# Performance work log

Measured on AMD Instinct MI355X. Metric: run time of the kernel, lower is better.

The kernel has to match this reference:

```python
import jax, jax.numpy as jnp
import numpy as np
from jax import lax

B, C, H, W = 4, 96, 256, 256
EPS = 1e-12  # torch F.normalize default eps


def setup_inputs() -> dict:
    key = jax.random.key(0)
    ks = jax.random.split(key, 7)
    s1 = 1.0 / np.sqrt(C).astype(np.float32)
    x = jax.random.normal(ks[0], (B, C, H, W), dtype=jnp.float32)
    qkv_w = jax.random.normal(ks[1], (3 * C, C), dtype=jnp.float32) * s1      # 1x1 conv as matmul
    qkv_b = jax.random.normal(ks[2], (3 * C,), dtype=jnp.float32) * 0.01
    dw_w = jax.random.normal(ks[3], (3 * C, 1, 3, 3), dtype=jnp.float32) / 3.0  # depthwise 3x3
    dw_b = jax.random.normal(ks[4], (3 * C,), dtype=jnp.float32) * 0.01
    temp = jnp.ones((C, 1, 1), dtype=jnp.float32)                             # nn.Parameter(ones(dim,1,1))
    proj_w = jax.random.normal(ks[5], (C, C), dtype=jnp.float32) * s1
    proj_b = jax.random.normal(ks[6], (C,), dtype=jnp.float32) * 0.01
    return {"x": x, "qkv_w": qkv_w, "qkv_b": qkv_b, "dw_w": dw_w,
            "dw_b": dw_b, "temp": temp, "proj_w": proj_w, "proj_b": proj_b}


def _l2norm_h(t):
    # torch F.normalize(t, dim=-2): L2 over the H axis, eps-clamped denominator
    n = jnp.sqrt(jnp.sum(t * t, axis=-2, keepdims=True))
    return t / jnp.maximum(n, EPS)


def reference(x, qkv_w, qkv_b, dw_w, dw_b, temp, proj_w, proj_b):
    # 1x1 conv QKV projection
    qkv = jnp.einsum('bchw,oc->bohw', x, qkv_w) + qkv_b[None, :, None, None]
    # depthwise 3x3 conv (groups = 3C), padding 1
    qkv = lax.conv_general_dilated(
        qkv, dw_w, window_strides=(1, 1), padding='SAME',
        feature_group_count=qkv.shape[1],
        dimension_numbers=('NCHW', 'OIHW', 'NCHW')) + dw_b[None, :, None, None]
    q, k, v = jnp.split(qkv, 3, axis=1)  # each [B,C,H,W]
    q1 = _l2norm_h(q)
    k1 = _l2norm_h(k)
    # attn1 = (q1^T @ k1) * temperature : [B,C,W,W], temp broadcasts over (W,W)
    attn = jnp.einsum('bchw,bchv->bcwv', q1, k1) * temp[None]
    attn = jax.nn.softmax(attn, axis=-2)
    # out = v @ attn : [B,C,H,W]
    out = jnp.einsum('bchw,bcwv->bchv', v, attn)
    # 1x1 output projection
    out = jnp.einsum('bchw,oc->bohw', out, proj_w) + proj_b[None, :, None, None]
    return out
```

## Files before the change

### kernel.cpp

```cpp
#include <hip/hip_runtime.h>

#define NC 96
#define NC3 288
#define NH 256
#define NW 256
#define NHW 65536

typedef unsigned short ushort_t;
typedef __attribute__((ext_vector_type(8))) short bf16x8;
typedef __attribute__((ext_vector_type(4))) float f32x4;

__device__ __forceinline__ ushort_t f2bf(float x) {
  unsigned u = __float_as_uint(x);
  u += 0x7fffu + ((u >> 16) & 1u);
  return (ushort_t)(u >> 16);
}
__device__ __forceinline__ float bf2f(ushort_t h) {
  return __uint_as_float((unsigned)h << 16);
}
__device__ __forceinline__ unsigned pack_split(float f) {
  unsigned u = __float_as_uint(f);
  unsigned ur = u + (0x7fffu + ((u >> 16) & 1u));
  const float rem = f - __uint_as_float(ur & 0xffff0000u);
  unsigned v = __float_as_uint(rem);
  v += 0x7fffu + ((v >> 16) & 1u);
  return (ur >> 16) | (v & 0xffff0000u);
}
__device__ __forceinline__ float upk(unsigned u) {
  return __uint_as_float(u << 16) + __uint_as_float(u & 0xffff0000u);
}

__global__ __launch_bounds__(256) void k_wprep(
    const float* __restrict__ qkv_w, const float* __restrict__ proj_w,
    ushort_t* __restrict__ wq_hi, ushort_t* __restrict__ wq_lo,
    ushort_t* __restrict__ wp_hi, ushort_t* __restrict__ wp_lo) {
  const int id = blockIdx.x * 256 + threadIdx.x;
  if (id < NC3 * NC) {
    const float v = qkv_w[id];
    const ushort_t h = f2bf(v);
    wq_hi[id] = h;
    wq_lo[id] = f2bf(v - bf2f(h));
  } else {
    const int j = id - NC3 * NC;
    const float v = proj_w[j];
    const ushort_t h = f2bf(v);
    wp_hi[j] = h;
    wp_lo[j] = f2bf(v - bf2f(h));
  }
}

template <int OUTC, bool TILED>
__global__ __launch_bounds__(256, 4) void k_conv(
    const float* __restrict__ in, const ushort_t* __restrict__ w_hi,
    const ushort_t* __restrict__ w_lo, const float* __restrict__ bias,
    float* __restrict__ out) {
  __shared__ __align__(16) char smem[39936];
  ushort_t* xh = (ushort_t*)smem;
  ushort_t* xl = (ushort_t*)(smem + 13312);
  float* xt48 = (float*)(smem + 26624);
  float* est = (float*)smem;
  const int t = threadIdx.x;
  const int bz = blockIdx.y;
  const int sblk = blockIdx.x;
  const int s0 = sblk * 64;
  const float* xb = in + (size_t)bz * NC * NHW + s0;

  const int lane = t & 63, wave = t >> 6;
  const int ln15 = lane & 15;
  const int akof = (lane >> 4) * 8;

#pragma unroll 1
  for (int half = 0; half < 2; ++half) {
    if (half) __syncthreads();
#pragma unroll
    for (int i = 0; i < 3; ++i) {
      const int idx = t + 256 * i;
      const int row = idx >> 4, c4 = (idx & 15) << 2;
      *(float4*)&xt48[row * 68 + c4] =
          *(const float4*)&xb[(size_t)(half * 48 + row) * NHW + c4];
    }
    __syncthreads();
    {
      const int s = t & 63, cg = t >> 6;
#pragma unroll
      for (int i = 0; i < 6; ++i) {
        const int cl = cg * 12 + i * 2;
        const float f0 = xt48[cl * 68 + s], f1 = xt48[(cl + 1) * 68 + s];
        const ushort_t h0 = f2bf(f0), h1 = f2bf(f1);
        const ushort_t l0 = f2bf(f0 - bf2f(h0)), l1 = f2bf(f1 - bf2f(h1));
        const int c = half * 48 + cl;
        *(unsigned*)&xh[s * 104 + c] = (unsigned)h0 | ((unsigned)h1 << 16);
        *(unsigned*)&xl[s * 104 + c] = (unsigned)l0 | ((unsigned)l1 << 16);
      }
    }
  }
  __syncthreads();
  bf16x8 bH[3], bL[3];
  {
    const int srow = wave * 16 + ln15;
#pragma unroll
    for (int kk = 0; kk < 3; ++kk) {
      bH[kk] = *(const bf16x8*)&xh[srow * 104 + kk * 32 + akof];
      bL[kk] = *(const bf16x8*)&xl[srow * 104 + kk * 32 + akof];
    }
  }

  constexpr int S = 3 * (OUTC / 96);
  const int sl = wave * 16 + ln15;
  f32x4 acc[6];
#pragma unroll
  for (int step = 0; step < S; ++step) {
    const int ocg = step / 3, kk = step % 3;
    if (kk == 0) {
#pragma unroll
      for (int m = 0; m < 6; ++m) acc[m] = (f32x4){0.f, 0.f, 0.f, 0.f};
    }
#pragma unroll
    for (int m = 0; m < 6; ++m) {
      const int wi = (ocg * 96 + m * 16 + ln15) * NC + kk * 32 + akof;
      const bf16x8 aH = *(const bf16x8*)(w_hi + wi);
      const bf16x8 aL = *(const bf16x8*)(w_lo + wi);
      acc[m] = __builtin_amdgcn_mfma_f32_16x16x32_bf16(aH, bH[kk], acc[m], 0, 0, 0);
      acc[m] = __builtin_amdgcn_mfma_f32_16x16x32_bf16(aH, bL[kk], acc[m], 0, 0, 0);
      acc[m] = __builtin_amdgcn_mfma_f32_16x16x32_bf16(aL, bH[kk], acc[m], 0, 0, 0);
    }
    if (kk == 2) {
      __syncthreads();
#pragma unroll
      for (int m = 0; m < 6; ++m) {
        const int o2 = m * 16 + (lane >> 4) * 4;
#pragma unroll
        for (int r = 0; r < 4; ++r) est[(o2 + r) * 66 + sl] = acc[m][r];
      }
      __syncthreads();
      if (TILED) {
        unsigned* ob = (unsigned*)out +
                       ((size_t)(bz * 1024 + sblk)) * OUTC * 64 +
                       (size_t)ocg * 96 * 64;
#pragma unroll
        for (int j = 0; j < 6; ++j) {
          const int idx = t + 256 * j;
          const int row = idx >> 4, c4 = (idx & 15) << 2;
          const float bs = bias[ocg * 96 + row];
          uint4 pkv;
          pkv.x = pack_split(est[row * 66 + c4 + 0] + bs);
          pkv.y = pack_split(est[row * 66 + c4 + 1] + bs);
          pkv.z = pack_split(est[row * 66 + c4 + 2] + bs);
          pkv.w = pack_split(est[row * 66 + c4 + 3] + bs);
          *(uint4*)(ob + (size_t)row * 64 + c4) = pkv;
        }
      } else {
        float* ob = out + (size_t)bz * OUTC * NHW + s0;
#pragma unroll
        for (int j = 0; j < 6; ++j) {
          const int idx = t + 256 * j;
          const int row = idx >> 4, c4 = (idx & 15) << 2;
          const float bs = bias[ocg * 96 + row];
          const float4 v = make_float4(
              est[row * 66 + c4] + bs, est[row * 66 + c4 + 1] + bs,
              est[row * 66 + c4 + 2] + bs, est[row * 66 + c4 + 3] + bs);
          *(float4*)(ob + (size_t)(ocg * 96 + row) * NHW + c4) = v;
        }
      }
    }
  }
}

__global__ __launch_bounds__(256, 8) void k_dw3(
    const unsigned* __restrict__ qkvt, const float* __restrict__ w,
    const float* __restrict__ bias, ushort_t* __restrict__ qt_hi,
    ushort_t* __restrict__ qt_lo, ushort_t* __restrict__ kt_hi,
    ushort_t* __restrict__ kt_lo, unsigned* __restrict__ v_pk,
    float* __restrict__ nq_p, float* __restrict__ nk_p) {
  __shared__ float sd[18][264];
  const int t = threadIdx.x;
  const int hb = blockIdx.x;
  const int bcc = blockIdx.y;
  const int b = bcc / NC3, ch = bcc % NC3;
  const int h0 = hb * 16;
  const unsigned* src = qkvt + (size_t)b * 1024 * NC3 * 64 + (size_t)ch * 64;
#pragma unroll
  for (int i = 0; i < 5; ++i) {
    const int idx = t + 256 * i;
    if (idx < 18 * 64) {
      const int r = idx >> 6, j = idx & 63;
      const int gh = h0 + r - 1;
      float4 v = make_float4(0.f, 0.f, 0.f, 0.f);
      if (gh >= 0 && gh < 256) {
        const int gw = 4 * j;
        const uint4 pv = *(const uint4*)&src[(size_t)(gh * 4 + (gw >> 6)) *
                                                 (NC3 * 64) +
                                             (gw & 63)];
        v = make_float4(upk(pv.x), upk(pv.y), upk(pv.z), upk(pv.w));
      }
      *(float4*)&sd[r][4 + 4 * j] = v;
    }
  }
  if (t < 36) {
    const int r = t >> 1;
    sd[r][(t & 1) ? 260 : 3] = 0.f;
  }
  __syncthreads();
  float wr[9];
#pragma unroll
  for (int k = 0; k < 9; ++k) wr[k] = w[ch * 9 + k];
  const float bs = bias[ch];
  const int wl = t;
  float res[16];
  float r0a = sd[0][wl + 3], r0b = sd[0][wl + 4], r0c = sd[0][wl + 5];
  float r1a = sd[1][wl + 3], r1b = sd[1][wl + 4], r1c = sd[1][wl + 5];
#pragma unroll
  for (int r = 0; r < 16; ++r) {
    const float r2a = sd[r + 2][wl + 3], r2b = sd[r + 2][wl + 4],
                r2c = sd[r + 2][wl + 5];
    float a = bs;
    a = fmaf(r0a, wr[0], a);
    a = fmaf(r0b, wr[1], a);
    a = fmaf(r0c, wr[2], a);
    a = fmaf(r1a, wr[3], a);
    a = fmaf(r1b, wr[4], a);
    a = fmaf(r1c, wr[5], a);
    a = fmaf(r2a, wr[6], a);
    a = fmaf(r2b, wr[7], a);
    a = fmaf(r2c, wr[8], a);
    res[r] = a;
    r0a = r1a; r0b = r1b; r0c = r1c;
    r1a = r2a; r1b = r2b; r1c = r2c;
  }
  if (ch < 192) {
    const int qk = ch / 96, c = ch - qk * 96;
    const int bc = b * 96 + c;
    float ss = 0.f;
#pragma unroll
    for (int r = 0; r < 16; ++r) ss = fmaf(res[r], res[r], ss);
    (qk ? nk_p : nq_p)[(size_t)bc * 4096 + hb * 256 + wl] = ss;
    const size_t tb = (size_t)bc * NHW + (size_t)hb * 4096 + (size_t)wl * 16;
    ushort_t* dh = (qk ? kt_hi : qt_hi) + tb;
    ushort_t* dl = (qk ? kt_lo : qt_lo) + tb;
#pragma unroll
    for (int j4 = 0; j4 < 2; ++j4) {
      uint4 H, L;
      unsigned* ph = (unsigned*)&H;
      unsigned* pl = (unsigned*)&L;
#pragma unroll
      for (int e = 0; e < 4; ++e) {
        const float f0 = res[j4 * 8 + 2 * e], f1 = res[j4 * 8 + 2 * e + 1];
        const ushort_t hh0 = f2bf(f0), hh1 = f2bf(f1);
        ph[e] = (unsigned)hh0 | ((unsigned)hh1 << 16);
        pl[e] = (unsigned)f2bf(f0 - bf2f(hh0)) |
                ((unsigned)f2bf(f1 - bf2f(hh1)) << 16);
      }
      *(uint4*)(dh + j4 * 8) = H;
      *(uint4*)(dl + j4 * 8) = L;
    }
  } else {
    const int bc = b * 96 + (ch - 192);
    const int wb = wl >> 5, wsub = wl & 31;
    unsigned* dp = v_pk + (size_t)bc * NHW + wb * 8192 + wsub;
#pragma unroll
    for (int r = 0; r < 16; ++r) {
      const float f = res[r];
      const ushort_t hh = f2bf(f);
      dp[(h0 + r) * 32] = (unsigned)hh | ((unsigned)f2bf(f - bf2f(hh)) << 16);
    }
  }
}

__global__ __launch_bounds__(256, 3) void k_attn_mfma(
    const ushort_t* __restrict__ qt_hi, const ushort_t* __restrict__ qt_lo,
    const ushort_t* __restrict__ kt_hi, const ushort_t* __restrict__ kt_lo,
    const float* __restrict__ nq_p, const float* __restrict__ nk_p,
    const float* __restrict__ temp, ushort_t* __restrict__ pt_hi,
    ushort_t* __restrict__ pt_lo) {
  __shared__ __align__(16) char smem[52480];
  ushort_t* qh = (ushort_t*)smem;
  ushort_t* ql = (ushort_t*)(smem + 20480);
  ushort_t* kh = (ushort_t*)(smem + 40960);
  ushort_t* kl = (ushort_t*)(smem + 46080);
  float* red = (float*)(smem + 51200);
  float* iqs = red;
  float* iks = (float*)(smem + 52224);
  ushort_t* pts = (ushort_t*)smem;

  const int t = threadIdx.x;
  const int lane = t & 63;
  const int wid = t >> 6;
  const int bid = blockIdx.x;
  const int pxb = gridDim.x >> 5;
  const int bc = (bid & 7) * pxb + (bid >> 5);
  const int v0 = ((bid >> 3) & 3) * 64;
  const size_t base_q = (size_t)bc * NHW;
  const size_t base_k = (size_t)bc * NHW;

  f32x4 acc[4][4];
#pragma unroll
  for (int mt = 0; mt < 4; ++mt)
#pragma unroll
    for (int nt = 0; nt < 4; ++nt) acc[mt][nt] = (f32x4){0.f, 0.f, 0.f, 0.f};

  for (int hb = 0; hb < 8; ++hb) {
    {
      const ushort_t* g0 = qt_hi + base_q + (size_t)(2 * hb) * 4096 + t * 16;
      const ushort_t* g1 = g0 + 4096;
      const ushort_t* gl0 = qt_lo + base_q + (size_t)(2 * hb) * 4096 + t * 16;
      const ushort_t* gl1 = gl0 + 4096;
      uint4* dh = (uint4*)(qh + t * 40);
      uint4* dl = (uint4*)(ql + t * 40);
      dh[0] = *(const uint4*)(g0);
      dh[1] = *(const uint4*)(g0 + 8);
      dh[2] = *(const uint4*)(g1);
      dh[3] = *(const uint4*)(g1 + 8);
      dl[0] = *(const uint4*)(gl0);
      dl[1] = *(const uint4*)(gl0 + 8);
      dl[2] = *(const uint4*)(gl1);
      dl[3] = *(const uint4*)(gl1 + 8);
      if (t < 64) {
        const ushort_t* k0 =
            kt_hi + base_k + (size_t)(2 * hb) * 4096 + (size_t)(v0 + t) * 16;
        const ushort_t* k1 = k0 + 4096;
        uint4* dk = (uint4*)(kh + t * 40);
        dk[0] = *(const uint4*)(k0);
        dk[1] = *(const uint4*)(k0 + 8);
        dk[2] = *(const uint4*)(k1);
        dk[3] = *(const uint4*)(k1 + 8);
      } else if (t < 128) {
        const int r = t - 64;
        const ushort_t* k0 =
            kt_lo + base_k + (size_t)(2 * hb) * 4096 + (size_t)(v0 + r) * 16;
        const ushort_t* k1 = k0 + 4096;
        uint4* dk = (uint4*)(kl + r * 40);
        dk[0] = *(const uint4*)(k0);
        dk[1] = *(const uint4*)(k0 + 8);
        dk[2] = *(const uint4*)(k1);
        dk[3] = *(const uint4*)(k1 + 8);
      }
    }
    __syncthreads();
    bf16x8 aH[4], aL[4];
#pragma unroll
    for (int mt = 0; mt < 4; ++mt) {
      const int off = (wid * 64 + mt * 16 + (lane & 15)) * 40 + (lane >> 4) * 8;
      aH[mt] = *(const bf16x8*)(qh + off);
      aL[mt] = *(const bf16x8*)(ql + off);
    }
#pragma unroll
    for (int nt = 0; nt < 4; ++nt) {
      const int off = (nt * 16 + (lane & 15)) * 40 + (lane >> 4) * 8;
      const bf16x8 bH = *(const bf16x8*)(kh + off);
      const bf16x8 bL = *(const bf16x8*)(kl + off);
#pragma unroll
      for (int mt = 0; mt < 4; ++mt) {
        acc[mt][nt] = __builtin_amdgcn_mfma_f32_16x16x32_bf16(aH[mt], bH, acc[mt][nt], 0, 0, 0);
        acc[mt][nt] = __builtin_amdgcn_mfma_f32_16x16x32_bf16(aH[mt], bL, acc[mt][nt], 0, 0, 0);
        acc[mt][nt] = __builtin_amdgcn_mfma_f32_16x16x32_bf16(aL[mt], bH, acc[mt][nt], 0, 0, 0);
      }
    }
    __syncthreads();
  }

  {
    float s8 = 0.f;
    const float* np = nq_p + (size_t)bc * 4096 + t;
#pragma unroll
    for (int hb = 0; hb < 16; ++hb) s8 += np[hb * 256];
    iqs[t] = 1.f / fmaxf(sqrtf(s8), 1e-12f);
    if (t < 64) {
      float sk8 = 0.f;
      const float* nk = nk_p + (size_t)bc * 4096 + v0 + t;
#pragma unroll
      for (int hb = 0; hb < 16; ++hb) sk8 += nk[hb * 256];
      iks[t] = temp[bc % NC] / fmaxf(sqrtf(sk8), 1e-12f);
    }
  }
  __syncthreads();
#pragma unroll
  for (int mt = 0; mt < 4; ++mt) {
    float iq4[4];
#pragma unroll
    for (int r = 0; r < 4; ++r)
      iq4[r] = iqs[wid * 64 + mt * 16 + (lane >> 4) * 4 + r];
#pragma unroll
    for (int nt = 0; nt < 4; ++nt) {
      const float ikv = iks[nt * 16 + (lane & 15)];
#pragma unroll
      for (int r = 0; r < 4; ++r) acc[mt][nt][r] *= iq4[r] * ikv;
    }
  }
  __syncthreads();

  float Mv[4], Sv[4];
#pragma unroll
  for (int nt = 0; nt < 4; ++nt) {
    float m = -3.4e38f;
#pragma unroll
    for (int mt = 0; mt < 4; ++mt)
#pragma unroll
      for (int r = 0; r < 4; ++r) m = fmaxf(m, acc[mt][nt][r]);
    m = fmaxf(m, __shfl_xor(m, 16));
    m = fmaxf(m, __shfl_xor(m, 32));
    if (lane < 16) red[wid * 64 + nt * 16 + lane] = m;
  }
  __syncthreads();
#pragma unroll
  for (int nt = 0; nt < 4; ++nt) {
    const int vl = nt * 16 + (lane & 15);
    Mv[nt] = fmaxf(fmaxf(red[vl], red[64 + vl]),
                   fmaxf(red[128 + vl], red[192 + vl]));
  }
  __syncthreads();
#pragma unroll
  for (int nt = 0; nt < 4; ++nt) {
    float s = 0.f;
#pragma unroll
    for (int mt = 0; mt < 4; ++mt)
#pragma unroll
      for (int r = 0; r < 4; ++r) {
        const float p = __expf(acc[mt][nt][r] - Mv[nt]);
        acc[mt][nt][r] = p;
        s += p;
      }
    s += __shfl_xor(s, 16);
    s += __shfl_xor(s, 32);
    if (lane < 16) red[wid * 64 + nt * 16 + lane] = s;
  }
  __syncthreads();
#pragma unroll
  for (int nt = 0; nt < 4; ++nt) {
    const int vl = nt * 16 + (lane & 15);
    Sv[nt] = 1.f / (red[vl] + red[64 + vl] + red[128 + vl] + red[192 + vl]);
  }
#pragma unroll
  for (int nt = 0; nt < 4; ++nt)
#pragma unroll
    for (int mt = 0; mt < 4; ++mt)
#pragma unroll
      for (int r = 0; r < 4; ++r) acc[mt][nt][r] *= Sv[nt];
  __syncthreads();

  for (int pass = 0; pass < 2; ++pass) {
#pragma unroll
    for (int nt = 0; nt < 4; ++nt)
#pragma unroll
      for (int mt = 0; mt < 4; ++mt) {
        ushort_t pk[4];
#pragma unroll
        for (int r = 0; r < 4; ++r) {
          const float p = acc[mt][nt][r];
          const ushort_t hi = f2bf(p);
          pk[r] = pass == 0 ? hi : f2bf(p - bf2f(hi));
        }
        const int v = nt * 16 + (lane & 15);
        const int wb2 = wid * 64 + mt * 16 + ((lane >> 4) << 2);
        *(ushort4*)(pts + v * 264 + wb2) =
            make_ushort4(pk[0], pk[1], pk[2], pk[3]);
      }
    __syncthreads();
    ushort_t* dst = pass == 0 ? pt_hi : pt_lo;
#pragma unroll
    for (int i = 0; i < 2; ++i) {
      const int cid = t + (i << 8);
      const int wb = cid >> 6, v = cid & 63;
      const ushort_t* sp = pts + v * 264 + wb * 32;
      ushort_t* d = dst + (size_t)bc * NHW + (size_t)wb * 8192 +
                    (size_t)(v0 + v) * 32;
#pragma unroll
      for (int j = 0; j < 4; ++j)
        *(uint4*)(d + j * 8) = *(const uint4*)(sp + j * 8);
    }
    __syncthreads();
  }
}

__global__ __launch_bounds__(256, 3) void k_av_mfma(
    const unsigned* __restrict__ v_pk, const ushort_t* __restrict__ pt_hi,
    const ushort_t* __restrict__ pt_lo, float* __restrict__ aout) {
  __shared__ __align__(16) ushort_t vh[128 * 40];
  __shared__ __align__(16) ushort_t vl[128 * 40];
  __shared__ __align__(16) ushort_t ph[128 * 40];
  __shared__ __align__(16) ushort_t pl[128 * 40];
  const int t = threadIdx.x;
  const int lane = t & 63;
  const int wid = t >> 6;
  const int bid = blockIdx.x;
  const int pxb = gridDim.x >> 5;
  const int bc = (bid & 7) * pxb + (bid >> 5);
  const int tile = (bid >> 3) & 3;
  const int h0 = (tile >> 1) * 128, v0 = (tile & 1) * 128;
  const int wh = wid >> 1, wv = wid & 1;

  f32x4 acc[4][4];
#pragma unroll
  for (int mt = 0; mt < 4; ++mt)
#pragma unroll
    for (int nt = 0; nt < 4; ++nt) acc[mt][nt] = (f32x4){0.f, 0.f, 0.f, 0.f};

  for (int wb = 0; wb < 8; ++wb) {
#pragma unroll
    for (int i = 0; i < 4; ++i) {
      const int id = t + (i << 8);
      const int row = id >> 3, q = id & 7;
      const uint4 pk = *(const uint4*)(v_pk + (size_t)bc * NHW + wb * 8192 +
                                       (size_t)(h0 + row) * 32 + q * 4);
      const ushort4 hi4 =
          make_ushort4((ushort_t)(pk.x & 0xffff), (ushort_t)(pk.y & 0xffff),
                       (ushort_t)(pk.z & 0xffff), (ushort_t)(pk.w & 0xffff));
      const ushort4 lo4 =
          make_ushort4((ushort_t)(pk.x >> 16), (ushort_t)(pk.y >> 16),
                       (ushort_t)(pk.z >> 16), (ushort_t)(pk.w >> 16));
      *(ushort4*)(vh + row * 40 + q * 4) = hi4;
      *(ushort4*)(vl + row * 40 + q * 4) = lo4;
    }
#pragma unroll
    for (int i = 0; i < 4; ++i) {
      const int id = t + (i << 8);
      const int arr = id >> 9, rem = id & 511;
      const int row = rem >> 2, q = rem & 3;
      const ushort_t* g = (arr ? pt_lo : pt_hi) + (size_t)bc * NHW +
                          wb * 8192 + (size_t)(v0 + row) * 32 + q * 8;
      ushort_t* d = (arr ? pl : ph) + row * 40 + q * 8;
      *(uint4*)d = *(const uint4*)g;
    }
    __syncthreads();
    bf16x8 aH[4], aL[4];
#pragma unroll
    for (int mt = 0; mt < 4; ++mt) {
      const int off = (wh * 64 + mt * 16 + (lane & 15)) * 40 + (lane >> 4) * 8;
      aH[mt] = *(const bf16x8*)(vh + off);
      aL[mt] = *(const bf16x8*)(vl + off);
    }
#pragma unroll
    for (int nt = 0; nt < 4; ++nt) {
      const int off = (wv * 64 + nt * 16 + (lane & 15)) * 40 + (lane >> 4) * 8;
      const bf16x8 bH = *(const bf16x8*)(ph + off);
      const bf16x8 bL = *(const bf16x8*)(pl + off);
#pragma unroll
      for (int mt = 0; mt < 4; ++mt) {
        acc[mt][nt] = __builtin_amdgcn_mfma_f32_16x16x32_bf16(aH[mt], bH, acc[mt][nt], 0, 0, 0);
        acc[mt][nt] = __builtin_amdgcn_mfma_f32_16x16x32_bf16(aH[mt], bL, acc[mt][nt], 0, 0, 0);
        acc[mt][nt] = __builtin_amdgcn_mfma_f32_16x16x32_bf16(aL[mt], bH, acc[mt][nt], 0, 0, 0);
      }
    }
    __syncthreads();
  }

#pragma unroll
  for (int mt = 0; mt < 4; ++mt) {
    const int hbase = h0 + wh * 64 + mt * 16 + ((lane >> 4) << 2);
#pragma unroll
    for (int nt = 0; nt < 4; ++nt) {
      const int vv = v0 + wv * 64 + nt * 16 + (lane & 15);
      float* o = aout + (size_t)bc * NHW + (size_t)hbase * NW + vv;
#pragma unroll
      for (int r = 0; r < 4; ++r) o[(size_t)r * NW] = acc[mt][nt][r];
    }
  }
}

extern "C" void kernel_launch(void* const* d_in, const int* in_sizes, int n_in,
                              void* d_out, int out_size, void* d_ws,
                              size_t ws_size, hipStream_t stream) {
  const float* x = (const float*)d_in[0];
  const float* qkv_w = (const float*)d_in[1];
  const float* qkv_b = (const float*)d_in[2];
  const float* dw_w = (const float*)d_in[3];
  const float* dw_b = (const float*)d_in[4];
  const float* temp = (const float*)d_in[5];
  const float* proj_w = (const float*)d_in[6];
  const float* proj_b = (const float*)d_in[7];
  float* out = (float*)d_out;

  auto need = [](int nb) -> size_t {
    return (size_t)nb * 154140672ull + 147456ull;
  };
  int nb = 1;
  if (need(4) <= ws_size) nb = 4;
  else if (need(2) <= ws_size) nb = 2;

  char* base = (char*)d_ws;
  const size_t QKV_T = (size_t)nb * 75497472ull;
  const size_t HALF = (size_t)nb * 12582912ull;
  const size_t NQB = (size_t)nb * 1572864ull;
  unsigned* qkv_tiled = (unsigned*)base;
  ushort_t* pt_hi = (ushort_t*)base;
  ushort_t* pt_lo = (ushort_t*)(base + HALF);
  float* aout = (float*)(base + 2 * HALF);
  char* p = base + QKV_T;
  ushort_t* qt_hi = (ushort_t*)p; p += HALF;
  ushort_t* qt_lo = (ushort_t*)p; p += HALF;
  ushort_t* kt_hi = (ushort_t*)p; p += HALF;
  ushort_t* kt_lo = (ushort_t*)p; p += HALF;
  unsigned* v_pk = (unsigned*)p; p += 2 * HALF;
  float* nq_p = (float*)p; p += NQB;
  float* nk_p = (float*)p; p += NQB;
  ushort_t* wq_hi = (ushort_t*)p; p += 55296;
  ushort_t* wq_lo = (ushort_t*)p; p += 55296;
  ushort_t* wp_hi = (ushort_t*)p; p += 18432;
  ushort_t* wp_lo = (ushort_t*)p;

  k_wprep<<<dim3(144), 256, 0, stream>>>(qkv_w, proj_w, wq_hi, wq_lo, wp_hi, wp_lo);

  const int BC = nb * NC;
  for (int b0 = 0; b0 < 4; b0 += nb) {
    const float* xb = x + (size_t)b0 * NC * NHW;
    float* outb = out + (size_t)b0 * NC * NHW;
    k_conv<NC3, true><<<dim3(1024, nb), 256, 0, stream>>>(
        xb, wq_hi, wq_lo, qkv_b, (float*)qkv_tiled);
    k_dw3<<<dim3(16, nb * NC3), 256, 0, stream>>>(
        qkv_tiled, dw_w, dw_b, qt_hi, qt_lo, kt_hi, kt_lo, v_pk, nq_p, nk_p);
    k_attn_mfma<<<dim3(BC * 4), 256, 0, stream>>>(
        qt_hi, qt_lo, kt_hi, kt_lo, nq_p, nk_p, temp, pt_hi, pt_lo);
    k_av_mfma<<<dim3(BC * 4), 256, 0, stream>>>(v_pk, pt_hi, pt_lo, aout);
    k_conv<NC, false><<<dim3(1024, nb), 256, 0, stream>>>(
        aout, wp_hi, wp_lo, proj_b, outb);
  }
}
```

Before: 519.7 us.

## Stage packed hi/lo weights in shared memory with register prefetch in 1x1 conv

Weights are now stored as one packed 32-bit word per element holding the bf16 hi and lo halves, instead of two separate bf16 arrays. Each conv step loads a 96x32 weight slab into shared memory, prefetches the next slab into registers, and unpacks the hi/lo fragments with byte permutes. Previously every wave read weight fragments straight from global memory. This removes redundant global loads across the four waves, at the cost of two extra barriers per step, more LDS, and permute instructions.

```diff
diff --git a/kernel.cpp b/kernel.cpp
--- a/kernel.cpp
+++ b/kernel.cpp
@@ -9,6 +9,7 @@
 typedef unsigned short ushort_t;
 typedef __attribute__((ext_vector_type(8))) short bf16x8;
 typedef __attribute__((ext_vector_type(4))) float f32x4;
+typedef __attribute__((ext_vector_type(4))) unsigned u32x4;
 
 __device__ __forceinline__ ushort_t f2bf(float x) {
   unsigned u = __float_as_uint(x);
@@ -30,33 +31,43 @@
   return __uint_as_float(u << 16) + __uint_as_float(u & 0xffff0000u);
 }
 
+union FragU {
+  u32x4 u;
+  bf16x8 b;
+};
+__device__ __forceinline__ void unpack8(const uint4 A, const uint4 B,
+                                        bf16x8& hf, bf16x8& lf) {
+  FragU H, L;
+  H.u = (u32x4){__builtin_amdgcn_perm(A.y, A.x, 0x05040100u),
+                __builtin_amdgcn_perm(A.w, A.z, 0x05040100u),
+                __builtin_amdgcn_perm(B.y, B.x, 0x05040100u),
+                __builtin_amdgcn_perm(B.w, B.z, 0x05040100u)};
+  L.u = (u32x4){__builtin_amdgcn_perm(A.y, A.x, 0x07060302u),
+                __builtin_amdgcn_perm(A.w, A.z, 0x07060302u),
+                __builtin_amdgcn_perm(B.y, B.x, 0x07060302u),
+                __builtin_amdgcn_perm(B.w, B.z, 0x07060302u)};
+  hf = H.b;
+  lf = L.b;
+}
+
 __global__ __launch_bounds__(256) void k_wprep(
     const float* __restrict__ qkv_w, const float* __restrict__ proj_w,
-    ushort_t* __restrict__ wq_hi, ushort_t* __restrict__ wq_lo,
-    ushort_t* __restrict__ wp_hi, ushort_t* __restrict__ wp_lo) {
+    unsigned* __restrict__ wq_pk, unsigned* __restrict__ wp_pk) {
   const int id = blockIdx.x * 256 + threadIdx.x;
-  if (id < NC3 * NC) {
-    const float v = qkv_w[id];
-    const ushort_t h = f2bf(v);
-    wq_hi[id] = h;
-    wq_lo[id] = f2bf(v - bf2f(h));
-  } else {
-    const int j = id - NC3 * NC;
-    const float v = proj_w[j];
-    const ushort_t h = f2bf(v);
-    wp_hi[j] = h;
-    wp_lo[j] = f2bf(v - bf2f(h));
-  }
+  if (id < NC3 * NC)
+    wq_pk[id] = pack_split(qkv_w[id]);
+  else
+    wp_pk[id - NC3 * NC] = pack_split(proj_w[id - NC3 * NC]);
 }
 
 template <int OUTC, bool TILED>
 __global__ __launch_bounds__(256, 4) void k_conv(
-    const float* __restrict__ in, const ushort_t* __restrict__ w_hi,
-    const ushort_t* __restrict__ w_lo, const float* __restrict__ bias,
-    float* __restrict__ out) {
-  __shared__ __align__(16) char smem[39936];
+    const float* __restrict__ in, const unsigned* __restrict__ w_pk,
+    const float* __restrict__ bias, float* __restrict__ out) {
+  __shared__ __align__(16) char smem[40448];
   ushort_t* xh = (ushort_t*)smem;
   ushort_t* xl = (ushort_t*)(smem + 13312);
+  unsigned* wpk = (unsigned*)(smem + 26624);
   float* xt48 = (float*)(smem + 26624);
   float* est = (float*)smem;
   const int t = threadIdx.x;
@@ -107,19 +118,43 @@
 
   constexpr int S = 3 * (OUTC / 96);
   const int sl = wave * 16 + ln15;
+  const int srow0 = t >> 3, scq = t & 7;
+  uint4 wreg[3];
+#pragma unroll
+  for (int i = 0; i < 3; ++i) {
+    const int row = srow0 + i * 32;
+    wreg[i] = *(const uint4*)(w_pk + (size_t)row * NC + scq * 4);
+  }
+
   f32x4 acc[6];
 #pragma unroll
   for (int step = 0; step < S; ++step) {
     const int ocg = step / 3, kk = step % 3;
+    __syncthreads();
+#pragma unroll
+    for (int i = 0; i < 3; ++i)
+      *(uint4*)&wpk[(srow0 + i * 32) * 36 + scq * 4] = wreg[i];
+    __syncthreads();
+    if (step + 1 < S) {
+      const int nocg = (step + 1) / 3, nkk = (step + 1) % 3;
+#pragma unroll
+      for (int i = 0; i < 3; ++i) {
+        const int row = srow0 + i * 32;
+        wreg[i] = *(const uint4*)(w_pk + (size_t)(nocg * 96 + row) * NC +
+                                  nkk * 32 + scq * 4);
+      }
+    }
     if (kk == 0) {
 #pragma unroll
       for (int m = 0; m < 6; ++m) acc[m] = (f32x4){0.f, 0.f, 0.f, 0.f};
     }
 #pragma unroll
     for (int m = 0; m < 6; ++m) {
-      const int wi = (ocg * 96 + m * 16 + ln15) * NC + kk * 32 + akof;
-      const bf16x8 aH = *(const bf16x8*)(w_hi + wi);
-      const bf16x8 aL = *(const bf16x8*)(w_lo + wi);
+      const int base = (m * 16 + ln15) * 36 + akof;
+      const uint4 A = *(const uint4*)&wpk[base];
+      const uint4 B = *(const uint4*)&wpk[base + 4];
+      bf16x8 aH, aL;
+      unpack8(A, B, aH, aL);
       acc[m] = __builtin_amdgcn_mfma_f32_16x16x32_bf16(aH, bH[kk], acc[m], 0, 0, 0);
       acc[m] = __builtin_amdgcn_mfma_f32_16x16x32_bf16(aH, bL[kk], acc[m], 0, 0, 0);
       acc[m] = __builtin_amdgcn_mfma_f32_16x16x32_bf16(aL, bH[kk], acc[m], 0, 0, 0);
@@ -592,25 +627,23 @@
   unsigned* v_pk = (unsigned*)p; p += 2 * HALF;
   float* nq_p = (float*)p; p += NQB;
   float* nk_p = (float*)p; p += NQB;
-  ushort_t* wq_hi = (ushort_t*)p; p += 55296;
-  ushort_t* wq_lo = (ushort_t*)p; p += 55296;
-  ushort_t* wp_hi = (ushort_t*)p; p += 18432;
-  ushort_t* wp_lo = (ushort_t*)p;
-
-  k_wprep<<<dim3(144), 256, 0, stream>>>(qkv_w, proj_w, wq_hi, wq_lo, wp_hi, wp_lo);
+  unsigned* wq_pk = (unsigned*)p; p += (size_t)NC3 * NC * 4;
+  unsigned* wp_pk = (unsigned*)p;
+
+  k_wprep<<<dim3(144), 256, 0, stream>>>(qkv_w, proj_w, wq_pk, wp_pk);
 
   const int BC = nb * NC;
   for (int b0 = 0; b0 < 4; b0 += nb) {
     const float* xb = x + (size_t)b0 * NC * NHW;
     float* outb = out + (size_t)b0 * NC * NHW;
     k_conv<NC3, true><<<dim3(1024, nb), 256, 0, stream>>>(
-        xb, wq_hi, wq_lo, qkv_b, (float*)qkv_tiled);
+        xb, wq_pk, qkv_b, (float*)qkv_tiled);
     k_dw3<<<dim3(16, nb * NC3), 256, 0, stream>>>(
         qkv_tiled, dw_w, dw_b, qt_hi, qt_lo, kt_hi, kt_lo, v_pk, nq_p, nk_p);
     k_attn_mfma<<<dim3(BC * 4), 256, 0, stream>>>(
         qt_hi, qt_lo, kt_hi, kt_lo, nq_p, nk_p, temp, pt_hi, pt_lo);
     k_av_mfma<<<dim3(BC * 4), 256, 0, stream>>>(v_pk, pt_hi, pt_lo, aout);
     k_conv<NC, false><<<dim3(1024, nb), 256, 0, stream>>>(
-        aout, wp_hi, wp_lo, proj_b, outb);
-  }
-}
+        aout, wp_pk, proj_b, outb);
+  }
+}
```

Measured after the change: 561.3 us. 8.0% more time.
